# Performance work log

Hardware: AMD Instinct MI355X
Metric: run time of the kernel (lower is better)

Reference implementation:

```python
import jax, jax.numpy as jnp
import numpy as np

B, N, P, K = 4, 8192, 2048, 16
C_IN, C_OUT, DIMS = 64, 128, 3
C_MID = C_OUT // 4                      # 32 (C_in != 0 branch)
DM = min(int(np.ceil(C_OUT / C_IN)), 4) # 2, depth multiplier for SepConv
C_DENSE = C_OUT // 2                    # 64, dense-projected feature dim
C_CAT = C_MID + C_DENSE                 # 96, lifted + projected features


def setup_inputs() -> dict:
    key = jax.random.key(0)
    ks = jax.random.split(key, 12)
    g = lambda k, shape, fan: jax.random.normal(k, shape, jnp.float32) / np.sqrt(fan).astype(np.float32)
    return {
        "pts": jax.random.normal(ks[0], (B, N, DIMS), jnp.float32),
        "fts": jax.random.normal(ks[1], (B, N, C_IN), jnp.float32),
        # PointCNN.dense: Linear(C_in, C_out//2) + ELU
        "dense_W": g(ks[2], (C_IN, C_DENSE), C_IN), "dense_b": jnp.zeros((C_DENSE,), jnp.float32),
        # XConv.dense1/dense2: Linear(dims,C_mid)+ELU, Linear(C_mid,C_mid)+ELU
        "d1_W": g(ks[3], (DIMS, C_MID), DIMS), "d1_b": jnp.zeros((C_MID,), jnp.float32),
        "d2_W": g(ks[4], (C_MID, C_MID), C_MID), "d2_b": jnp.zeros((C_MID,), jnp.float32),
        # conv2d: Conv2d(dims, K*K, (1,K)) + ELU, weight (out, in, kW)
        "conv_W": g(ks[5], (K * K, DIMS, K), DIMS * K), "conv_b": jnp.zeros((K * K,), jnp.float32),
        # dep_conv1/2: depthwise Conv2d(K, K*K, (1,K), groups=K); weight (group, mult, kW)
        "dw1_W": g(ks[6], (K, K, K), K), "dw1_b": jnp.zeros((K, K), jnp.float32),
        "dw2_W": g(ks[7], (K, K, K), K), "dw2_b": jnp.zeros((K, K), jnp.float32),
        # end_conv SepConv: depthwise (C_CAT groups, DM mult, (1,K)) then pointwise 1x1 -> C_OUT, ELU
        "sep_dw_W": g(ks[8], (C_CAT, DM, K), K), "sep_dw_b": jnp.zeros((C_CAT, DM), jnp.float32),
        "sep_pw_W": g(ks[9], (C_OUT, C_CAT, DM), C_CAT * DM), "sep_pw_b": jnp.zeros((C_OUT,), jnp.float32),
    }


def _fps(pts, npoint):
    """Iterative farthest point sampling (deterministic start at index 0)."""
    b, n, _ = pts.shape
    dist0 = jnp.full((b, n), 1e10, pts.dtype)
    far0 = jnp.zeros((b,), jnp.int32)

    def step(carry, _):
        dist, far = carry
        centroid = jnp.take_along_axis(pts, far[:, None, None], axis=1)  # [B,1,3]
        d = jnp.sum((pts - centroid) ** 2, -1)                            # [B,N]
        dist = jnp.minimum(dist, d)
        return (dist, jnp.argmax(dist, -1).astype(jnp.int32)), far

    _, idx = jax.lax.scan(step, (dist0, far0), None, length=npoint)  # [P,B]
    idx = idx.T                                                       # [B,P]
    return jnp.take_along_axis(pts, idx[..., None], axis=1)          # [B,P,3]


def reference(pts, fts, dense_W, dense_b, d1_W, d1_b, d2_W, d2_b,
              conv_W, conv_b, dw1_W, dw1_b, dw2_W, dw2_b,
              sep_dw_W, sep_dw_b, sep_pw_W, sep_pw_b):
    rep_pts = _fps(pts, P)                                            # [B,P,3]
    fts_d = jax.nn.elu(fts @ dense_W + dense_b)                       # [B,N,64]
    # KNN: squared distances rep->all points, K smallest
    d2 = (jnp.sum(rep_pts ** 2, -1)[..., None]
          - 2.0 * jnp.einsum('npc,nqc->npq', rep_pts, pts)
          + jnp.sum(pts ** 2, -1)[:, None, :])                        # [B,P,N]
    _, idx = jax.lax.top_k(-d2, K)                                    # [B,P,K]
    bidx = jnp.arange(B)[:, None, None]
    pts_reg = pts[bidx, idx]                                          # [B,P,K,3]
    fts_reg = fts_d[bidx, idx]                                        # [B,P,K,64]
    # XConv
    pl = pts_reg - rep_pts[:, :, None, :]                             # local coords
    lift = jax.nn.elu(jax.nn.elu(pl @ d1_W + d1_b) @ d2_W + d2_b)     # [B,P,K,C_MID]
    fts_cat = jnp.concatenate([lift, fts_reg], -1)                    # [B,P,K,C_CAT]
    X = jax.nn.elu(jnp.einsum('npkc,ock->npo', pl, conv_W) + conv_b).reshape(B, P, K, K)
    # depthwise convs over neighbor axis (spatial dim collapses to 1 -> einsum)
    X = jax.nn.elu(jnp.einsum('npij,jmi->npjm', X, dw1_W) + dw1_b)
    X = jnp.einsum('npij,jmi->npjm', X, dw2_W) + dw2_b
    fts_X = jnp.einsum('npab,npbc->npac', X, fts_cat)                 # [B,P,K,C_CAT]
    # separable end conv: depthwise over K, pointwise to C_OUT, ELU
    d = jnp.einsum('npkc,cmk->npcm', fts_X, sep_dw_W) + sep_dw_b
    fts_p = jax.nn.elu(jnp.einsum('npcm,ocm->npo', d, sep_pw_W) + sep_pw_b)  # [B,P,C_OUT]
    return rep_pts, fts_p
```

## Files before the change

kernel.cpp:

```cpp
#include <hip/hip_runtime.h>

#define BB 4
#define NN 8192
#define PP 2048
#define KNB 16
#define CIN 64
#define COUT 128

__device__ __forceinline__ float elu(float x) { return x > 0.0f ? x : expm1f(x); }

__device__ __forceinline__ unsigned fkey(float d) {
    unsigned u = __float_as_uint(d);
    unsigned m = (unsigned)((int)u >> 31);
    return u ^ (m | 0x80000000u);
}

__device__ __forceinline__ float wave_max_dpp(float v) {
#define DPP_STEP(ctrl)                                                         \
    {                                                                          \
        int x = __float_as_int(v);                                             \
        int y = __builtin_amdgcn_update_dpp(x, x, (ctrl), 0xf, 0xf, false);    \
        v = fmaxf(v, __int_as_float(y));                                       \
    }
    DPP_STEP(0x111)
    DPP_STEP(0x112)
    DPP_STEP(0x114)
    DPP_STEP(0x118)
    DPP_STEP(0x142)
    DPP_STEP(0x143)
#undef DPP_STEP
    return __int_as_float(__builtin_amdgcn_readlane(__float_as_int(v), 63));
}

__device__ __forceinline__ unsigned wave_min_u32_dpp(unsigned v) {
#define DPP_STEP(ctrl)                                                         \
    {                                                                          \
        int y = __builtin_amdgcn_update_dpp((int)v, (int)v, (ctrl), 0xf, 0xf, false); \
        v = min(v, (unsigned)y);                                               \
    }
    DPP_STEP(0x111)
    DPP_STEP(0x112)
    DPP_STEP(0x114)
    DPP_STEP(0x118)
    DPP_STEP(0x142)
    DPP_STEP(0x143)
#undef DPP_STEP
    return (unsigned)__builtin_amdgcn_readlane((int)v, 63);
}

#define PREP_BLOCKS 64
#define DENSE_BASE (4 + PREP_BLOCKS)
#define TOTAL_BLOCKS (DENSE_BASE + BB * NN / 8)

__global__ __launch_bounds__(512) void fps_kernel(
    const float* __restrict__ pts, float* __restrict__ rep,
    const float* __restrict__ fts, const float* __restrict__ denseW,
    const float* __restrict__ denseb, float* __restrict__ ftsd,
    const float* __restrict__ convW, const float* __restrict__ dw1W,
    const float* __restrict__ dw2W, const float* __restrict__ sdwW,
    const float* __restrict__ spwW,
    float* __restrict__ convT, float* __restrict__ dw1T, float* __restrict__ dw2T,
    float* __restrict__ sdwT, float* __restrict__ spwT, float* __restrict__ ptsT) {
    const int bid = blockIdx.x;
    const int t = threadIdx.x;

    __shared__ float spx[NN];
    __shared__ float spy[NN];
    __shared__ float spz[NN];
    __shared__ unsigned long long partk[2][8];

    if (bid >= DENSE_BASE) {
        const int row = (bid - DENSE_BASE) * 8 + (t >> 6);
        const int c = t & 63;
        float v = fts[(size_t)row * 64 + c];
        float acc = denseb[c];
#pragma unroll 8
        for (int k = 0; k < 64; ++k) acc = fmaf(__shfl(v, k), denseW[k * 64 + c], acc);
        ftsd[(size_t)row * 64 + c] = elu(acc);
        return;
    }
    if (bid >= 4) {
        int i = (bid - 4) * 512 + t;
        if (i < 12288) {
            int k = i & 15, c = (i >> 4) % 3, o = i / 48;
            convT[(c * 16 + k) * 256 + o] = convW[i];
        }
        if (i < 4096) {
            int ii = i & 15, e = i >> 4;
            dw1T[ii * 256 + e] = dw1W[i];
            dw2T[ii * 256 + e] = dw2W[i];
        }
        if (i < 3072) {
            int k = i & 15, e = i >> 4;
            sdwT[k * 192 + e] = sdwW[i];
        }
        if (i < 24576) {
            int e2 = i % 192, o = i / 192;
            spwT[e2 * 128 + o] = spwW[i];
        }
        {
            int j = i & 8191, b2 = i >> 13;
#pragma unroll
            for (int d = 0; d < 3; ++d)
                ptsT[((size_t)b2 * 3 + d) * NN + j] = pts[((size_t)b2 * NN + j) * 3 + d];
        }
        return;
    }

    __builtin_amdgcn_s_setprio(1);

    const int b = bid;
    const int lane = t & 63, wave = t >> 6;

    const float* pb = pts + (size_t)b * NN * 3;
    for (int i = t; i < NN; i += 512) {
        spx[i] = pb[3 * i + 0];
        spy[i] = pb[3 * i + 1];
        spz[i] = pb[3 * i + 2];
    }
    __syncthreads();

    float px[16], py[16], pz[16], dist[16];
#pragma unroll
    for (int r = 0; r < 16; ++r) {
        px[r] = spx[t * 16 + r];
        py[r] = spy[t * 16 + r];
        pz[r] = spz[t * 16 + r];
        dist[r] = 1e10f;
    }

    float cx = spx[0], cy = spy[0], cz = spz[0];
    if (t == 0) {
        rep[(size_t)b * PP * 3 + 0] = cx;
        rep[(size_t)b * PP * 3 + 1] = cy;
        rep[(size_t)b * PP * 3 + 2] = cz;
    }

    int buf = 0;
    for (int s = 1; s < PP; ++s) {
        float bv = -1.0f; int bi = 0;
#pragma unroll
        for (int r = 0; r < 16; ++r) {
            float dx = __fsub_rn(px[r], cx);
            float dy = __fsub_rn(py[r], cy);
            float dz = __fsub_rn(pz[r], cz);
            float d = __fadd_rn(__fadd_rn(__fmul_rn(dx, dx), __fmul_rn(dy, dy)), __fmul_rn(dz, dz));
            float nd = fminf(dist[r], d);
            dist[r] = nd;
            bool tk = nd > bv;
            bi = tk ? (t * 16 + r) : bi;
            bv = fmaxf(nd, bv);
        }

        float wmax = wave_max_dpp(bv);
        unsigned long long mask = __ballot(bv == wmax);
        int wl = __ffsll(mask) - 1;
        int wbi = __shfl(bi, wl);

        if (lane == 0)
            partk[buf][wave] = ((unsigned long long)__float_as_uint(wmax) << 32)
                             | (unsigned)(8191 - wbi);
        __syncthreads();

        unsigned long long kk = partk[buf][0];
#pragma unroll
        for (int q = 1; q < 8; ++q) {
            unsigned long long c = partk[buf][q];
            kk = c > kk ? c : kk;
        }
        int widx = 8191 - (int)(unsigned)(kk & 0xFFFFFFFFULL);
        cx = spx[widx]; cy = spy[widx]; cz = spz[widx];
        if (t == 0) {
            float* rp = rep + ((size_t)b * PP + s) * 3;
            rp[0] = cx; rp[1] = cy; rp[2] = cz;
        }
        buf ^= 1;
    }
}

__global__ __launch_bounds__(256) void knn_kernel(const float* __restrict__ ptsT,
                                                  const float* __restrict__ rep,
                                                  int* __restrict__ kidx) {
    const int wid = blockIdx.x * 4 + (threadIdx.x >> 6);
    const int lane = threadIdx.x & 63;
    const int b = wid >> 11;
    const float* pxT = ptsT + (size_t)b * 3 * NN;
    const float* pyT = pxT + NN;
    const float* pzT = pxT + 2 * NN;

    float rx = rep[(size_t)wid * 3 + 0];
    float ry = rep[(size_t)wid * 3 + 1];
    float rz = rep[(size_t)wid * 3 + 2];
    float a = __fadd_rn(__fadd_rn(__fmul_rn(rx, rx), __fmul_rn(ry, ry)), __fmul_rn(rz, rz));

    unsigned long long key[16];
#pragma unroll
    for (int s = 0; s < 16; ++s) key[s] = ~0ULL;

    unsigned tau = 0xFFFFFFFFu;
    int it = 0;
    for (int j = lane; j < NN; j += 64, ++it) {
        float qx = pxT[j], qy = pyT[j], qz = pzT[j];
        float cc = __fadd_rn(__fadd_rn(__fmul_rn(qx, qx), __fmul_rn(qy, qy)), __fmul_rn(qz, qz));
        float bs = __fadd_rn(__fadd_rn(__fmul_rn(rx, qx), __fmul_rn(ry, qy)), __fmul_rn(rz, qz));
        float d2 = __fadd_rn(__fsub_rn(a, __fmul_rn(2.0f, bs)), cc);
        unsigned fk = fkey(d2);
        if (fk <= tau) {
            unsigned long long nk = ((unsigned long long)fk << 32) | (unsigned)j;
            if (nk < key[15]) {
                key[15] = nk;
#pragma unroll
                for (int s2 = 15; s2 > 0; --s2) {
                    unsigned long long u = key[s2 - 1], w = key[s2];
                    bool sw = w < u;
                    key[s2 - 1] = sw ? w : u;
                    key[s2] = sw ? u : w;
                }
            }
        }
        if ((it & 7) == 7)
            tau = wave_min_u32_dpp((unsigned)(key[15] >> 32));
    }

    int outv = 0;
#pragma unroll 1
    for (int r = 0; r < 16; ++r) {
        unsigned long long h = key[0];
#pragma unroll
        for (int off = 1; off < 64; off <<= 1) {
            unsigned long long o = __shfl_xor(h, off);
            h = (o < h) ? o : h;
        }
        if (lane == r) outv = (int)(unsigned)(h & 0xFFFFFFFFull);
        if (key[0] == h) {
#pragma unroll
            for (int s2 = 0; s2 < 15; ++s2) key[s2] = key[s2 + 1];
            key[15] = ~0ULL;
        }
    }
    if (lane < 16) kidx[(size_t)wid * 16 + lane] = outv;
}

__global__ __launch_bounds__(128) void xconv_kernel(
    const float* __restrict__ pts, const float* __restrict__ rep,
    const float* __restrict__ ftsd, const int* __restrict__ kidx,
    const float* __restrict__ d1W, const float* __restrict__ d1b,
    const float* __restrict__ d2W, const float* __restrict__ d2b,
    const float* __restrict__ convT, const float* __restrict__ convb,
    const float* __restrict__ dw1T, const float* __restrict__ dw1b,
    const float* __restrict__ dw2T, const float* __restrict__ dw2b,
    const float* __restrict__ sdwT, const float* __restrict__ sdwb,
    const float* __restrict__ spwT, const float* __restrict__ spwb,
    float* __restrict__ outp) {
    const int bp = blockIdx.x;
    const int b = bp >> 11;
    const int t = threadIdx.x;
    const int c64 = t & 63;

    __shared__ float pl[16][3];
    __shared__ int nidx[16];
    __shared__ float fcat[16][96];
    __shared__ float A1[16][32];
    __shared__ float Xm[16][17];
    __shared__ float X2[16][17];
    __shared__ float X3[16][17];
    __shared__ float fX[16][97];
    __shared__ float dsep[192];

    if (t < 16) {
        int id = kidx[(size_t)bp * 16 + t];
        nidx[t] = id;
        const float* q = pts + ((size_t)b * NN + id) * 3;
        const float* rr = rep + (size_t)bp * 3;
        pl[t][0] = q[0] - rr[0];
        pl[t][1] = q[1] - rr[1];
        pl[t][2] = q[2] - rr[2];
    }
    __syncthreads();

#pragma unroll
    for (int it = 0; it < 8; ++it) {
        int k = (t >> 6) + it * 2;
        fcat[k][32 + c64] = ftsd[((size_t)b * NN + nidx[k]) * 64 + c64];
    }

#pragma unroll
    for (int r2 = 0; r2 < 4; ++r2) {
        int e = t + 128 * r2; int k = e >> 5, j = e & 31;
        float acc = d1b[j];
        acc = fmaf(pl[k][0], d1W[j], acc);
        acc = fmaf(pl[k][1], d1W[32 + j], acc);
        acc = fmaf(pl[k][2], d1W[64 + j], acc);
        A1[k][j] = elu(acc);
    }
    __syncthreads();

#pragma unroll
    for (int r2 = 0; r2 < 4; ++r2) {
        int e = t + 128 * r2; int k = e >> 5, j = e & 31;
        float acc = d2b[j];
#pragma unroll
        for (int c = 0; c < 32; ++c) acc = fmaf(A1[k][c], d2W[c * 32 + j], acc);
        fcat[k][j] = elu(acc);
    }
    __syncthreads();

    {
        float a0 = convb[t], a1 = convb[t + 128];
#pragma unroll
        for (int c = 0; c < 3; ++c)
#pragma unroll
            for (int k = 0; k < 16; ++k) {
                float p = pl[k][c];
                const float* w = convT + (c * 16 + k) * 256 + t;
                a0 = fmaf(p, w[0],   a0);
                a1 = fmaf(p, w[128], a1);
            }
        Xm[t >> 4][t & 15] = elu(a0);
        Xm[(t >> 4) + 8][t & 15] = elu(a1);
    }
    __syncthreads();

    {
        int m = t & 15, j0 = t >> 4;
        float a0 = dw1b[t], a1 = dw1b[t + 128];
#pragma unroll
        for (int i = 0; i < 16; ++i) {
            const float* w = dw1T + i * 256 + t;
            a0 = fmaf(Xm[i][j0],     w[0],   a0);
            a1 = fmaf(Xm[i][j0 + 8], w[128], a1);
        }
        X2[j0][m] = elu(a0); X2[j0 + 8][m] = elu(a1);
    }
    __syncthreads();

    {
        int m = t & 15, j0 = t >> 4;
        float a0 = dw2b[t], a1 = dw2b[t + 128];
#pragma unroll
        for (int i = 0; i < 16; ++i) {
            const float* w = dw2T + i * 256 + t;
            a0 = fmaf(X2[i][j0],     w[0],   a0);
            a1 = fmaf(X2[i][j0 + 8], w[128], a1);
        }
        X3[j0][m] = a0; X3[j0 + 8][m] = a1;
    }
    __syncthreads();

#pragma unroll
    for (int r2 = 0; r2 < 12; ++r2) {
        int e = t + 128 * r2; int a = e & 15, c = e >> 4;
        float acc = 0.0f;
#pragma unroll
        for (int q = 0; q < 16; ++q) acc = fmaf(X3[a][q], fcat[q][c], acc);
        fX[a][c] = acc;
    }
    __syncthreads();

#pragma unroll
    for (int r2 = 0; r2 < 2; ++r2) {
        int e = t + 128 * r2;
        if (e < 192) {
            int c = e >> 1;
            float acc = sdwb[e];
#pragma unroll
            for (int k = 0; k < 16; ++k) acc = fmaf(fX[k][c], sdwT[k * 192 + e], acc);
            dsep[e] = acc;
        }
    }
    __syncthreads();

    {
        float a0 = spwb[t];
#pragma unroll 16
        for (int e2 = 0; e2 < 192; ++e2)
            a0 = fmaf(dsep[e2], spwT[e2 * 128 + t], a0);
        outp[(size_t)bp * 128 + t] = elu(a0);
    }
}

extern "C" void kernel_launch(void* const* d_in, const int* in_sizes, int n_in,
                              void* d_out, int out_size, void* d_ws, size_t ws_size,
                              hipStream_t stream) {
    const float* pts    = (const float*)d_in[0];
    const float* fts    = (const float*)d_in[1];
    const float* denseW = (const float*)d_in[2];
    const float* denseb = (const float*)d_in[3];
    const float* d1W    = (const float*)d_in[4];
    const float* d1b    = (const float*)d_in[5];
    const float* d2W    = (const float*)d_in[6];
    const float* d2b    = (const float*)d_in[7];
    const float* convW  = (const float*)d_in[8];
    const float* convb  = (const float*)d_in[9];
    const float* dw1W   = (const float*)d_in[10];
    const float* dw1b   = (const float*)d_in[11];
    const float* dw2W   = (const float*)d_in[12];
    const float* dw2b   = (const float*)d_in[13];
    const float* sdwW   = (const float*)d_in[14];
    const float* sdwb   = (const float*)d_in[15];
    const float* spwW   = (const float*)d_in[16];
    const float* spwb   = (const float*)d_in[17];

    float* rep  = (float*)d_out;
    float* outp = (float*)d_out + (size_t)BB * PP * 3;

    float* ftsd = (float*)d_ws;
    int*   kidx = (int*)((char*)d_ws + (size_t)BB * NN * CIN * sizeof(float));
    float* wts  = (float*)((char*)d_ws + (size_t)BB * NN * CIN * sizeof(float)
                                       + (size_t)BB * PP * KNB * sizeof(int));
    float* convT = wts;
    float* dw1T  = wts + 12288;
    float* dw2T  = wts + 16384;
    float* sdwT  = wts + 20480;
    float* spwT  = wts + 23552;
    float* ptsT  = wts + 48128;

    fps_kernel<<<TOTAL_BLOCKS, 512, 0, stream>>>(pts, rep, fts, denseW, denseb, ftsd,
                                                 convW, dw1W, dw2W, sdwW, spwW,
                                                 convT, dw1T, dw2T, sdwT, spwT, ptsT);
    knn_kernel<<<BB * PP / 4, 256, 0, stream>>>(ptsT, rep, kidx);
    xconv_kernel<<<BB * PP, 128, 0, stream>>>(pts, rep, ftsd, kidx,
                                              d1W, d1b, d2W, d2b, convT, convb,
                                              dw1T, dw1b, dw2T, dw2b,
                                              sdwT, sdwb, spwT, spwb, outp);
}
```

Baseline: 2.274 ms.

## Split FPS into chunks and overlap kNN+XConv of earlier chunks

The farthest-point sampling loop is split into four launches of 512 steps each, with the per-point min-distance state saved to and restored from global memory between launches. In launches 2-4 the spare blocks run a fused kNN + XConv pipeline on the representative points finished in the previous chunk, so the idle GPU overlaps with the serial FPS. Only the final chunk's kNN and XConv run after FPS completes. The costs are extra launches, state save and restore, a larger shared-memory union, and possible interference with the FPS blocks despite their raised priority.

```diff
diff --git a/kernel.cpp b/kernel.cpp
--- a/kernel.cpp
+++ b/kernel.cpp
@@ -6,6 +6,7 @@
 #define KNB 16
 #define CIN 64
 #define COUT 128
+#define CHUNK 512
 
 __device__ __forceinline__ float elu(float x) { return x > 0.0f ? x : expm1f(x); }
 
@@ -22,12 +23,8 @@
         int y = __builtin_amdgcn_update_dpp(x, x, (ctrl), 0xf, 0xf, false);    \
         v = fmaxf(v, __int_as_float(y));                                       \
     }
-    DPP_STEP(0x111)
-    DPP_STEP(0x112)
-    DPP_STEP(0x114)
-    DPP_STEP(0x118)
-    DPP_STEP(0x142)
-    DPP_STEP(0x143)
+    DPP_STEP(0x111) DPP_STEP(0x112) DPP_STEP(0x114)
+    DPP_STEP(0x118) DPP_STEP(0x142) DPP_STEP(0x143)
 #undef DPP_STEP
     return __int_as_float(__builtin_amdgcn_readlane(__float_as_int(v), 63));
 }
@@ -38,21 +35,34 @@
         int y = __builtin_amdgcn_update_dpp((int)v, (int)v, (ctrl), 0xf, 0xf, false); \
         v = min(v, (unsigned)y);                                               \
     }
-    DPP_STEP(0x111)
-    DPP_STEP(0x112)
-    DPP_STEP(0x114)
-    DPP_STEP(0x118)
-    DPP_STEP(0x142)
-    DPP_STEP(0x143)
+    DPP_STEP(0x111) DPP_STEP(0x112) DPP_STEP(0x114)
+    DPP_STEP(0x118) DPP_STEP(0x142) DPP_STEP(0x143)
 #undef DPP_STEP
     return (unsigned)__builtin_amdgcn_readlane((int)v, 63);
 }
 
+struct FpsSmem {
+    float spx[NN], spy[NN], spz[NN];
+    unsigned long long partk[2][8];
+};
+struct ConsSmem {
+    int kidx[8][16];
+    float pl[4][16][3];
+    int nidx[4][16];
+    float fcat[4][16][96];
+    float A1[4][16][32];
+    float Xm[4][16][17];
+    float X2[4][16][17];
+    float X3[4][16][17];
+    float fX[4][16][97];
+    float dsep[4][192];
+};
+union Smem { FpsSmem fps; ConsSmem cons; };
+
 #define PREP_BLOCKS 64
 #define DENSE_BASE (4 + PREP_BLOCKS)
-#define TOTAL_BLOCKS (DENSE_BASE + BB * NN / 8)
-
-__global__ __launch_bounds__(512) void fps_kernel(
+
+__global__ __launch_bounds__(512) void mega_kernel(
     const float* __restrict__ pts, float* __restrict__ rep,
     const float* __restrict__ fts, const float* __restrict__ denseW,
     const float* __restrict__ denseb, float* __restrict__ ftsd,
@@ -60,26 +70,30 @@
     const float* __restrict__ dw2W, const float* __restrict__ sdwW,
     const float* __restrict__ spwW,
     float* __restrict__ convT, float* __restrict__ dw1T, float* __restrict__ dw2T,
-    float* __restrict__ sdwT, float* __restrict__ spwT, float* __restrict__ ptsT) {
+    float* __restrict__ sdwT, float* __restrict__ spwT, float* __restrict__ ptsT,
+    float* __restrict__ fstate,
+    const float* __restrict__ d1W, const float* __restrict__ d1b,
+    const float* __restrict__ d2W, const float* __restrict__ d2b,
+    const float* __restrict__ convb, const float* __restrict__ dw1b,
+    const float* __restrict__ dw2b, const float* __restrict__ sdwb,
+    const float* __restrict__ spwb, float* __restrict__ outp,
+    int s0, int s1, int mode, int cons_p0) {
     const int bid = blockIdx.x;
     const int t = threadIdx.x;
 
-    __shared__ float spx[NN];
-    __shared__ float spy[NN];
-    __shared__ float spz[NN];
-    __shared__ unsigned long long partk[2][8];
-
-    if (bid >= DENSE_BASE) {
-        const int row = (bid - DENSE_BASE) * 8 + (t >> 6);
-        const int c = t & 63;
-        float v = fts[(size_t)row * 64 + c];
-        float acc = denseb[c];
+    __shared__ Smem sm;
+
+    if (bid >= 4 && mode == 0) {
+        if (bid >= DENSE_BASE) {
+            const int row = (bid - DENSE_BASE) * 8 + (t >> 6);
+            const int c = t & 63;
+            float v = fts[(size_t)row * 64 + c];
+            float acc = denseb[c];
 #pragma unroll 8
-        for (int k = 0; k < 64; ++k) acc = fmaf(__shfl(v, k), denseW[k * 64 + c], acc);
-        ftsd[(size_t)row * 64 + c] = elu(acc);
-        return;
-    }
-    if (bid >= 4) {
+            for (int k = 0; k < 64; ++k) acc = fmaf(__shfl(v, k), denseW[k * 64 + c], acc);
+            ftsd[(size_t)row * 64 + c] = elu(acc);
+            return;
+        }
         int i = (bid - 4) * 512 + t;
         if (i < 12288) {
             int k = i & 15, c = (i >> 4) % 3, o = i / 48;
@@ -107,6 +121,196 @@
         return;
     }
 
+    if (bid >= 4) {
+        const int cb = bid - 4;
+        const int wv = t >> 6, lane = t & 63;
+
+        {
+            const int gp = cb * 8 + wv;
+            const int b = gp >> 9;
+            const int p = cons_p0 + (gp & 511);
+            const int wid = b * PP + p;
+            const float* pxT = ptsT + (size_t)b * 3 * NN;
+            const float* pyT = pxT + NN;
+            const float* pzT = pxT + 2 * NN;
+
+            float rx = rep[(size_t)wid * 3 + 0];
+            float ry = rep[(size_t)wid * 3 + 1];
+            float rz = rep[(size_t)wid * 3 + 2];
+            float a = __fadd_rn(__fadd_rn(__fmul_rn(rx, rx), __fmul_rn(ry, ry)), __fmul_rn(rz, rz));
+
+            unsigned long long key[16];
+#pragma unroll
+            for (int s = 0; s < 16; ++s) key[s] = ~0ULL;
+
+            unsigned tau = 0xFFFFFFFFu;
+            int it = 0;
+            for (int j = lane; j < NN; j += 64, ++it) {
+                float qx = pxT[j], qy = pyT[j], qz = pzT[j];
+                float cc = __fadd_rn(__fadd_rn(__fmul_rn(qx, qx), __fmul_rn(qy, qy)), __fmul_rn(qz, qz));
+                float bs = __fadd_rn(__fadd_rn(__fmul_rn(rx, qx), __fmul_rn(ry, qy)), __fmul_rn(rz, qz));
+                float d2 = __fadd_rn(__fsub_rn(a, __fmul_rn(2.0f, bs)), cc);
+                unsigned fk = fkey(d2);
+                if (fk <= tau) {
+                    unsigned long long nk = ((unsigned long long)fk << 32) | (unsigned)j;
+                    if (nk < key[15]) {
+                        key[15] = nk;
+#pragma unroll
+                        for (int s2 = 15; s2 > 0; --s2) {
+                            unsigned long long u = key[s2 - 1], w = key[s2];
+                            bool sw = w < u;
+                            key[s2 - 1] = sw ? w : u;
+                            key[s2] = sw ? u : w;
+                        }
+                    }
+                }
+                if ((it & 7) == 7)
+                    tau = wave_min_u32_dpp((unsigned)(key[15] >> 32));
+            }
+
+            int outv = 0;
+#pragma unroll 1
+            for (int r = 0; r < 16; ++r) {
+                unsigned long long h = key[0];
+#pragma unroll
+                for (int off = 1; off < 64; off <<= 1) {
+                    unsigned long long o = __shfl_xor(h, off);
+                    h = (o < h) ? o : h;
+                }
+                if (lane == r) outv = (int)(unsigned)(h & 0xFFFFFFFFull);
+                if (key[0] == h) {
+#pragma unroll
+                    for (int s2 = 0; s2 < 15; ++s2) key[s2] = key[s2 + 1];
+                    key[15] = ~0ULL;
+                }
+            }
+            if (lane < 16) sm.cons.kidx[wv][lane] = outv;
+        }
+        __syncthreads();
+
+        const int g = t >> 7, tl = t & 127, c64 = tl & 63;
+#pragma unroll 1
+        for (int pp = 0; pp < 2; ++pp) {
+            const int pi = g * 2 + pp;
+            const int gp2 = cb * 8 + pi;
+            const int b = gp2 >> 9;
+            const int bp = b * PP + cons_p0 + (gp2 & 511);
+            __syncthreads();
+
+            if (tl < 16) {
+                int id = sm.cons.kidx[pi][tl];
+                sm.cons.nidx[g][tl] = id;
+                const float* q = pts + ((size_t)b * NN + id) * 3;
+                const float* rr = rep + (size_t)bp * 3;
+                sm.cons.pl[g][tl][0] = q[0] - rr[0];
+                sm.cons.pl[g][tl][1] = q[1] - rr[1];
+                sm.cons.pl[g][tl][2] = q[2] - rr[2];
+            }
+            __syncthreads();
+
+#pragma unroll
+            for (int it = 0; it < 8; ++it) {
+                int k = (tl >> 6) + it * 2;
+                sm.cons.fcat[g][k][32 + c64] = ftsd[((size_t)b * NN + sm.cons.nidx[g][k]) * 64 + c64];
+            }
+
+#pragma unroll
+            for (int r2 = 0; r2 < 4; ++r2) {
+                int e = tl + 128 * r2; int k = e >> 5, j = e & 31;
+                float acc = d1b[j];
+                acc = fmaf(sm.cons.pl[g][k][0], d1W[j], acc);
+                acc = fmaf(sm.cons.pl[g][k][1], d1W[32 + j], acc);
+                acc = fmaf(sm.cons.pl[g][k][2], d1W[64 + j], acc);
+                sm.cons.A1[g][k][j] = elu(acc);
+            }
+            __syncthreads();
+
+#pragma unroll
+            for (int r2 = 0; r2 < 4; ++r2) {
+                int e = tl + 128 * r2; int k = e >> 5, j = e & 31;
+                float acc = d2b[j];
+#pragma unroll
+                for (int c = 0; c < 32; ++c) acc = fmaf(sm.cons.A1[g][k][c], d2W[c * 32 + j], acc);
+                sm.cons.fcat[g][k][j] = elu(acc);
+            }
+            __syncthreads();
+
+            {
+                float a0 = convb[tl], a1 = convb[tl + 128];
+#pragma unroll
+                for (int c = 0; c < 3; ++c)
+#pragma unroll
+                    for (int k = 0; k < 16; ++k) {
+                        float p2 = sm.cons.pl[g][k][c];
+                        const float* w = convT + (c * 16 + k) * 256 + tl;
+                        a0 = fmaf(p2, w[0],   a0);
+                        a1 = fmaf(p2, w[128], a1);
+                    }
+                sm.cons.Xm[g][tl >> 4][tl & 15] = elu(a0);
+                sm.cons.Xm[g][(tl >> 4) + 8][tl & 15] = elu(a1);
+            }
+            __syncthreads();
+
+            {
+                int m = tl & 15, j0 = tl >> 4;
+                float a0 = dw1b[tl], a1 = dw1b[tl + 128];
+#pragma unroll
+                for (int i = 0; i < 16; ++i) {
+                    const float* w = dw1T + i * 256 + tl;
+                    a0 = fmaf(sm.cons.Xm[g][i][j0],     w[0],   a0);
+                    a1 = fmaf(sm.cons.Xm[g][i][j0 + 8], w[128], a1);
+                }
+                sm.cons.X2[g][j0][m] = elu(a0); sm.cons.X2[g][j0 + 8][m] = elu(a1);
+            }
+            __syncthreads();
+
+            {
+                int m = tl & 15, j0 = tl >> 4;
+                float a0 = dw2b[tl], a1 = dw2b[tl + 128];
+#pragma unroll
+                for (int i = 0; i < 16; ++i) {
+                    const float* w = dw2T + i * 256 + tl;
+                    a0 = fmaf(sm.cons.X2[g][i][j0],     w[0],   a0);
+                    a1 = fmaf(sm.cons.X2[g][i][j0 + 8], w[128], a1);
+                }
+                sm.cons.X3[g][j0][m] = a0; sm.cons.X3[g][j0 + 8][m] = a1;
+            }
+            __syncthreads();
+
+#pragma unroll
+            for (int r2 = 0; r2 < 12; ++r2) {
+                int e = tl + 128 * r2; int a = e & 15, c = e >> 4;
+                float acc = 0.0f;
+#pragma unroll
+                for (int q = 0; q < 16; ++q) acc = fmaf(sm.cons.X3[g][a][q], sm.cons.fcat[g][q][c], acc);
+                sm.cons.fX[g][a][c] = acc;
+            }
+            __syncthreads();
+
+#pragma unroll
+            for (int r2 = 0; r2 < 2; ++r2) {
+                int e = tl + 128 * r2;
+                if (e < 192) {
+                    int c = e >> 1;
+                    float acc = sdwb[e];
+#pragma unroll
+                    for (int k = 0; k < 16; ++k) acc = fmaf(sm.cons.fX[g][k][c], sdwT[k * 192 + e], acc);
+                    sm.cons.dsep[g][e] = acc;
+                }
+            }
+            __syncthreads();
+
+            {
+                float a0 = spwb[tl];
+#pragma unroll 16
+                for (int e2 = 0; e2 < 192; ++e2)
+                    a0 = fmaf(sm.cons.dsep[g][e2], spwT[e2 * 128 + tl], a0);
+                outp[(size_t)bp * 128 + tl] = elu(a0);
+            }
+        }
+        return;
+    }
+
     __builtin_amdgcn_s_setprio(1);
 
     const int b = bid;
@@ -114,30 +318,39 @@
 
     const float* pb = pts + (size_t)b * NN * 3;
     for (int i = t; i < NN; i += 512) {
-        spx[i] = pb[3 * i + 0];
-        spy[i] = pb[3 * i + 1];
-        spz[i] = pb[3 * i + 2];
+        sm.fps.spx[i] = pb[3 * i + 0];
+        sm.fps.spy[i] = pb[3 * i + 1];
+        sm.fps.spz[i] = pb[3 * i + 2];
     }
     __syncthreads();
 
     float px[16], py[16], pz[16], dist[16];
 #pragma unroll
     for (int r = 0; r < 16; ++r) {
-        px[r] = spx[t * 16 + r];
-        py[r] = spy[t * 16 + r];
-        pz[r] = spz[t * 16 + r];
-        dist[r] = 1e10f;
-    }
-
-    float cx = spx[0], cy = spy[0], cz = spz[0];
-    if (t == 0) {
-        rep[(size_t)b * PP * 3 + 0] = cx;
-        rep[(size_t)b * PP * 3 + 1] = cy;
-        rep[(size_t)b * PP * 3 + 2] = cz;
+        px[r] = sm.fps.spx[t * 16 + r];
+        py[r] = sm.fps.spy[t * 16 + r];
+        pz[r] = sm.fps.spz[t * 16 + r];
+    }
+
+    float cx, cy, cz;
+    if (s0 == 1) {
+#pragma unroll
+        for (int r = 0; r < 16; ++r) dist[r] = 1e10f;
+        cx = sm.fps.spx[0]; cy = sm.fps.spy[0]; cz = sm.fps.spz[0];
+        if (t == 0) {
+            rep[(size_t)b * PP * 3 + 0] = cx;
+            rep[(size_t)b * PP * 3 + 1] = cy;
+            rep[(size_t)b * PP * 3 + 2] = cz;
+        }
+    } else {
+#pragma unroll
+        for (int r = 0; r < 16; ++r) dist[r] = fstate[((size_t)b * 16 + r) * 512 + t];
+        const float* rp = rep + ((size_t)b * PP + s0 - 1) * 3;
+        cx = rp[0]; cy = rp[1]; cz = rp[2];
     }
 
     int buf = 0;
-    for (int s = 1; s < PP; ++s) {
+    for (int s = s0; s < s1; ++s) {
         float bv = -1.0f; int bi = 0;
 #pragma unroll
         for (int r = 0; r < 16; ++r) {
@@ -158,32 +371,38 @@
         int wbi = __shfl(bi, wl);
 
         if (lane == 0)
-            partk[buf][wave] = ((unsigned long long)__float_as_uint(wmax) << 32)
-                             | (unsigned)(8191 - wbi);
+            sm.fps.partk[buf][wave] = ((unsigned long long)__float_as_uint(wmax) << 32)
+                                    | (unsigned)(8191 - wbi);
         __syncthreads();
 
-        unsigned long long kk = partk[buf][0];
+        unsigned long long kk = sm.fps.partk[buf][0];
 #pragma unroll
         for (int q = 1; q < 8; ++q) {
-            unsigned long long c = partk[buf][q];
+            unsigned long long c = sm.fps.partk[buf][q];
             kk = c > kk ? c : kk;
         }
         int widx = 8191 - (int)(unsigned)(kk & 0xFFFFFFFFULL);
-        cx = spx[widx]; cy = spy[widx]; cz = spz[widx];
+        cx = sm.fps.spx[widx]; cy = sm.fps.spy[widx]; cz = sm.fps.spz[widx];
         if (t == 0) {
             float* rp = rep + ((size_t)b * PP + s) * 3;
             rp[0] = cx; rp[1] = cy; rp[2] = cz;
         }
         buf ^= 1;
     }
+
+    if (s1 < PP) {
+#pragma unroll
+        for (int r = 0; r < 16; ++r) fstate[((size_t)b * 16 + r) * 512 + t] = dist[r];
+    }
 }
 
 __global__ __launch_bounds__(256) void knn_kernel(const float* __restrict__ ptsT,
                                                   const float* __restrict__ rep,
-                                                  int* __restrict__ kidx) {
-    const int wid = blockIdx.x * 4 + (threadIdx.x >> 6);
+                                                  int* __restrict__ kidx, int p_base) {
+    const int wl_ = blockIdx.x * 4 + (threadIdx.x >> 6);
     const int lane = threadIdx.x & 63;
-    const int b = wid >> 11;
+    const int b = wl_ >> 9;
+    const int wid = b * PP + p_base + (wl_ & 511);
     const float* pxT = ptsT + (size_t)b * 3 * NN;
     const float* pyT = pxT + NN;
     const float* pzT = pxT + 2 * NN;
@@ -251,9 +470,10 @@
     const float* __restrict__ dw2T, const float* __restrict__ dw2b,
     const float* __restrict__ sdwT, const float* __restrict__ sdwb,
     const float* __restrict__ spwT, const float* __restrict__ spwb,
-    float* __restrict__ outp) {
-    const int bp = blockIdx.x;
-    const int b = bp >> 11;
+    float* __restrict__ outp, int p_base) {
+    const int bl = blockIdx.x;
+    const int b = bl >> 9;
+    const int bp = b * PP + p_base + (bl & 511);
     const int t = threadIdx.x;
     const int c64 = t & 63;
 
@@ -408,19 +628,29 @@
     int*   kidx = (int*)((char*)d_ws + (size_t)BB * NN * CIN * sizeof(float));
     float* wts  = (float*)((char*)d_ws + (size_t)BB * NN * CIN * sizeof(float)
                                        + (size_t)BB * PP * KNB * sizeof(int));
-    float* convT = wts;
-    float* dw1T  = wts + 12288;
-    float* dw2T  = wts + 16384;
-    float* sdwT  = wts + 20480;
-    float* spwT  = wts + 23552;
-    float* ptsT  = wts + 48128;
-
-    fps_kernel<<<TOTAL_BLOCKS, 512, 0, stream>>>(pts, rep, fts, denseW, denseb, ftsd,
-                                                 convW, dw1W, dw2W, sdwW, spwW,
-                                                 convT, dw1T, dw2T, sdwT, spwT, ptsT);
-    knn_kernel<<<BB * PP / 4, 256, 0, stream>>>(ptsT, rep, kidx);
-    xconv_kernel<<<BB * PP, 128, 0, stream>>>(pts, rep, ftsd, kidx,
-                                              d1W, d1b, d2W, d2b, convT, convb,
-                                              dw1T, dw1b, dw2T, dw2b,
-                                              sdwT, sdwb, spwT, spwb, outp);
+    float* convT  = wts;
+    float* dw1T   = wts + 12288;
+    float* dw2T   = wts + 16384;
+    float* sdwT   = wts + 20480;
+    float* spwT   = wts + 23552;
+    float* ptsT   = wts + 48128;
+    float* fstate = wts + 146432;
+
+    mega_kernel<<<DENSE_BASE + BB * NN / 8, 512, 0, stream>>>(
+        pts, rep, fts, denseW, denseb, ftsd, convW, dw1W, dw2W, sdwW, spwW,
+        convT, dw1T, dw2T, sdwT, spwT, ptsT, fstate,
+        d1W, d1b, d2W, d2b, convb, dw1b, dw2b, sdwb, spwb, outp,
+        1, CHUNK, 0, 0);
+    for (int k = 1; k < 4; ++k) {
+        mega_kernel<<<4 + 256, 512, 0, stream>>>(
+            pts, rep, fts, denseW, denseb, ftsd, convW, dw1W, dw2W, sdwW, spwW,
+            convT, dw1T, dw2T, sdwT, spwT, ptsT, fstate,
+            d1W, d1b, d2W, d2b, convb, dw1b, dw2b, sdwb, spwb, outp,
+            k * CHUNK, (k + 1) * CHUNK, 1, (k - 1) * CHUNK);
+    }
+    knn_kernel<<<512, 256, 0, stream>>>(ptsT, rep, kidx, 3 * CHUNK);
+    xconv_kernel<<<2048, 128, 0, stream>>>(pts, rep, ftsd, kidx,
+                                           d1W, d1b, d2W, d2b, convT, convb,
+                                           dw1T, dw1b, dw2T, dw2b,
+                                           sdwT, sdwb, spwT, spwb, outp, 3 * CHUNK);
 }
```

Measured after the change: 2.243 ms. No clear change (-1.4%).
